# Kernel tuning notes

Hardware: AMD Instinct MI355X
Metric: run time of the kernel (lower is better)

## Reference

```python
import jax, jax.numpy as jnp
import numpy as np

L, B, E, H = 1024, 8, 1024, 16
HD = E // H
SCALE = HD ** -0.5
EPS = 1e-5


def setup_inputs() -> dict:
    key = jax.random.key(0)
    ks = jax.random.split(key, 6)
    s = E ** -0.5
    return {
        "x": jax.random.normal(ks[0], (L, B, E), dtype=jnp.float32),
        "attn_mask": jnp.zeros((L, L), dtype=jnp.float32),
        "Wq": jax.random.normal(ks[1], (E, E), dtype=jnp.float32) * s,
        "bq": jnp.zeros((E,), dtype=jnp.float32),
        "Wk": jax.random.normal(ks[2], (E, E), dtype=jnp.float32) * s,
        "bk": jnp.zeros((E,), dtype=jnp.float32),
        "Wv": jax.random.normal(ks[3], (E, E), dtype=jnp.float32) * s,
        "bv": jnp.zeros((E,), dtype=jnp.float32),
        "Wo": jax.random.normal(ks[4], (E, E), dtype=jnp.float32) * s,
        "bo": jnp.zeros((E,), dtype=jnp.float32),
        "gamma": jnp.ones((E,), dtype=jnp.float32),
        "beta": jnp.zeros((E,), dtype=jnp.float32),
    }


def _layernorm(x, gamma, beta):
    mu = jnp.mean(x, axis=-1, keepdims=True)
    var = jnp.mean(jnp.square(x - mu), axis=-1, keepdims=True)
    return (x - mu) * jax.lax.rsqrt(var + EPS) * gamma + beta


def reference(x, attn_mask, Wq, bq, Wk, bk, Wv, bv, Wo, bo, gamma, beta):
    # x: (L, B, E); pre-LN residual attention block (dropout=0, eval)
    ln_x = _layernorm(x, gamma, beta)
    # torch Linear: y = x @ W.T + b
    q = (ln_x @ Wq.T + bq) * SCALE
    k = ln_x @ Wk.T + bk
    v = ln_x @ Wv.T + bv
    # (L, B, E) -> (B, H, L, hd)
    def split_heads(t):
        return t.reshape(L, B, H, HD).transpose(1, 2, 0, 3)
    q, k, v = split_heads(q), split_heads(k), split_heads(v)
    # full attention matrix, as in the original non-fused bmm path
    attn = jnp.einsum('bhqd,bhkd->bhqk', q, k) + attn_mask[None, None]
    attn = jax.nn.softmax(attn, axis=-1)
    out = jnp.einsum('bhqk,bhkd->bhqd', attn, v)  # (B, H, L, hd)
    out = out.transpose(2, 0, 1, 3).reshape(L, B, E)
    out = out @ Wo.T + bo
    return x + out
```

## Files before the change

### kernel.cpp

```cpp
#include <hip/hip_runtime.h>

#define LL 1024
#define BB 8
#define EE 1024
#define HH 16
#define HD 64
#define MROWS (LL*BB)

typedef __attribute__((ext_vector_type(8))) short short8v;
typedef __attribute__((ext_vector_type(4))) float f32x4;
typedef __attribute__((ext_vector_type(16))) float f32x16;

#define LOG2E 1.44269504088896f

__device__ __forceinline__ unsigned short tobf(float f) {
    union { float f; unsigned u; } un; un.f = f;
    unsigned u = un.u;
    u += 0x7fffu + ((u >> 16) & 1u);
    return (unsigned short)(u >> 16);
}

__device__ __forceinline__ float max3f(float a, float b, float c) {
    return fmaxf(fmaxf(a, b), c);
}

__device__ __forceinline__ void load_lds16(const unsigned short* g, unsigned short* l) {
    __builtin_amdgcn_global_load_lds((const __attribute__((address_space(1))) unsigned int*)g,
                                     (__attribute__((address_space(3))) unsigned int*)l,
                                     16, 0, 0);
}

__global__ __launch_bounds__(256) void convw4_kernel(const float* __restrict__ w0,
                                                     const float* __restrict__ w1,
                                                     const float* __restrict__ w2,
                                                     const float* __restrict__ w3,
                                                     unsigned short* __restrict__ o0,
                                                     unsigned short* __restrict__ o1,
                                                     unsigned short* __restrict__ o2,
                                                     unsigned short* __restrict__ o3) {
    const float* w; unsigned short* o;
    switch (blockIdx.y) {
        case 0:  w = w0; o = o0; break;
        case 1:  w = w1; o = o1; break;
        case 2:  w = w2; o = o2; break;
        default: w = w3; o = o3; break;
    }
    int i = (blockIdx.x * 256 + threadIdx.x) * 4;
    float4 v = *(const float4*)&w[i];
    ushort4 r;
    r.x = tobf(v.x); r.y = tobf(v.y); r.z = tobf(v.z); r.w = tobf(v.w);
    *(ushort4*)&o[i] = r;
}

__global__ __launch_bounds__(256) void maskprep_kernel(const float* __restrict__ m,
                                                       unsigned* __restrict__ o,
                                                       unsigned* __restrict__ flag) {
    __shared__ float t_sh[64][65];
    const int q0 = blockIdx.x * 64, k0 = blockIdx.y * 64;
    const int tid = threadIdx.x;
    unsigned nz = 0;
    {
        const int r = tid >> 2, c0 = (tid & 3) * 16;
        #pragma unroll
        for (int i = 0; i < 4; ++i) {
            float4 v = *(const float4*)&m[(size_t)(q0 + r) * LL + k0 + c0 + i*4];
            nz |= (v.x != 0.0f) | (v.y != 0.0f) | (v.z != 0.0f) | (v.w != 0.0f);
            t_sh[r][c0+i*4+0] = v.x; t_sh[r][c0+i*4+1] = v.y;
            t_sh[r][c0+i*4+2] = v.z; t_sh[r][c0+i*4+3] = v.w;
        }
    }
    if (__any(nz) && (tid & 63) == 0) atomicOr(flag, 1u);
    __syncthreads();
    const int k2l = tid >> 3, qi = (tid & 7) * 8;
    unsigned pk[8];
    #pragma unroll
    for (int j = 0; j < 8; ++j) {
        const unsigned lo = tobf(t_sh[qi+j][2*k2l]   * LOG2E);
        const unsigned hb = tobf(t_sh[qi+j][2*k2l+1] * LOG2E);
        pk[j] = lo | (hb << 16);
    }
    unsigned* orow = &o[(size_t)(k0/2 + k2l) * LL + q0 + qi];
    *(uint4*)&orow[0] = make_uint4(pk[0], pk[1], pk[2], pk[3]);
    *(uint4*)&orow[4] = make_uint4(pk[4], pk[5], pk[6], pk[7]);
}

__global__ __launch_bounds__(256) void ln_kernel(const float* __restrict__ x,
                                                 const float* __restrict__ gamma,
                                                 const float* __restrict__ beta,
                                                 unsigned short* __restrict__ out) {
    const int row = blockIdx.x;
    const int tid = threadIdx.x;
    const float4 v = *(const float4*)&x[(size_t)row * EE + tid * 4];
    float s = v.x + v.y + v.z + v.w;
    float q = v.x*v.x + v.y*v.y + v.z*v.z + v.w*v.w;
    #pragma unroll
    for (int off = 1; off < 64; off <<= 1) {
        s += __shfl_xor(s, off);
        q += __shfl_xor(q, off);
    }
    __shared__ float ss[4], sq[4];
    const int wv = tid >> 6;
    if ((tid & 63) == 0) { ss[wv] = s; sq[wv] = q; }
    __syncthreads();
    s = ss[0] + ss[1] + ss[2] + ss[3];
    q = sq[0] + sq[1] + sq[2] + sq[3];
    const float mu = s * (1.0f / EE);
    const float var = q * (1.0f / EE) - mu * mu;
    const float rs = rsqrtf(var + 1e-5f);
    ushort4 o;
    o.x = tobf((v.x - mu) * rs * gamma[tid*4+0] + beta[tid*4+0]);
    o.y = tobf((v.y - mu) * rs * gamma[tid*4+1] + beta[tid*4+1]);
    o.z = tobf((v.z - mu) * rs * gamma[tid*4+2] + beta[tid*4+2]);
    o.w = tobf((v.w - mu) * rs * gamma[tid*4+3] + beta[tid*4+3]);
    *(ushort4*)&out[(size_t)row * EE + tid * 4] = o;
}

#define GEMM128_BODY(A_, W_)                                                              \
    __shared__ unsigned short a_sh[3][128*32];                                            \
    __shared__ unsigned short b_sh[3][128*32];                                            \
    const int tid = threadIdx.x, lane = tid & 63, wave = tid >> 6;                        \
    const int bm = blockIdx.y * 128, bn = blockIdx.x * 128;                               \
    const int wr = (wave >> 1) * 64, wc = (wave & 1) * 64;                                \
    const int l16 = lane & 15, q4 = lane >> 4;                                            \
    const int grow = lane >> 2;                                                           \
    const int gswz = (((lane & 3) ^ (grow & 3)) * 8);                                     \
    const int rslot = (q4 ^ (l16 & 3)) * 16;                       \
    f32x4 acc[4][4] = {};                                                                 \
    _Pragma("unroll")                                                                     \
    for (int i = 0; i < 2; ++i) {                                                         \
        const int ch = wave * 2 + i;                                                      \
        load_lds16(&A_[(size_t)(bm + ch*16 + grow)*EE + gswz], &a_sh[0][ch*512]);         \
        load_lds16(&W_[(size_t)(bn + ch*16 + grow)*EE + gswz], &b_sh[0][ch*512]);         \
    }                                                                                     \
    _Pragma("unroll")                                                                     \
    for (int i = 0; i < 2; ++i) {                                                         \
        const int ch = wave * 2 + i;                                                      \
        load_lds16(&A_[(size_t)(bm + ch*16 + grow)*EE + 32 + gswz], &a_sh[1][ch*512]);    \
        load_lds16(&W_[(size_t)(bn + ch*16 + grow)*EE + 32 + gswz], &b_sh[1][ch*512]);    \
    }                                                                                     \
    int buf = 0, sb = 2;                                                                  \
    for (int it = 0; it < 32; ++it) {                                                     \
        if (it < 31) asm volatile("s_waitcnt vmcnt(4)" ::: "memory");                     \
        else         asm volatile("s_waitcnt vmcnt(0)" ::: "memory");                     \
        __builtin_amdgcn_s_barrier();                                                     \
        if (it < 30) {                                                                    \
            const int kn = (it + 2) * 32;                                                 \
            _Pragma("unroll")                                                             \
            for (int i = 0; i < 2; ++i) {                                                 \
                const int ch = wave * 2 + i;                                              \
                load_lds16(&A_[(size_t)(bm + ch*16 + grow)*EE + kn + gswz], &a_sh[sb][ch*512]); \
                load_lds16(&W_[(size_t)(bn + ch*16 + grow)*EE + kn + gswz], &b_sh[sb][ch*512]); \
            }                                                                             \
        }                                                                                 \
        short8v af[4], bf[4];                                                             \
        _Pragma("unroll")                                                                 \
        for (int mi = 0; mi < 4; ++mi)                                                    \
            af[mi] = *(const short8v*)((const char*)&a_sh[buf][0] + (size_t)(wr + mi*16 + l16)*64 + rslot); \
        _Pragma("unroll")                                                                 \
        for (int ni = 0; ni < 4; ++ni)                                                    \
            bf[ni] = *(const short8v*)((const char*)&b_sh[buf][0] + (size_t)(wc + ni*16 + l16)*64 + rslot); \
        __builtin_amdgcn_s_setprio(1);                                                    \
        _Pragma("unroll")                                                                 \
        for (int mi = 0; mi < 4; ++mi)                                                    \
            _Pragma("unroll")                                                             \
            for (int ni = 0; ni < 4; ++ni)                                                \
                acc[mi][ni] = __builtin_amdgcn_mfma_f32_16x16x32_bf16(af[mi], bf[ni], acc[mi][ni], 0, 0, 0); \
        __builtin_amdgcn_s_setprio(0);                                                    \
        buf = (buf == 2) ? 0 : buf + 1;                                                   \
        sb  = (sb  == 2) ? 0 : sb  + 1;                                                   \
    }

__global__ __launch_bounds__(256) void gemm_qkv(const unsigned short* __restrict__ A,
                                                const unsigned short* __restrict__ W,
                                                const float* __restrict__ bq,
                                                const float* __restrict__ bk,
                                                const float* __restrict__ bv,
                                                unsigned short* __restrict__ qo,
                                                unsigned short* __restrict__ ko,
                                                unsigned short* __restrict__ vo) {
    GEMM128_BODY(A, W)
    const int seg = blockIdx.x >> 3;
    const float* bias = seg == 0 ? bq : (seg == 1 ? bk : bv);
    #pragma unroll
    for (int mi = 0; mi < 4; ++mi) {
        #pragma unroll
        for (int ni = 0; ni < 4; ++ni) {
            #pragma unroll
            for (int r = 0; r < 4; ++r) {
                const int m  = bm + wr + mi*16 + (lane >> 4)*4 + r;
                const int nn = (bn & 1023) + wc + ni*16 + l16;
                const float v = acc[mi][ni][r] + bias[nn];
                const int l = m >> 3, b = m & 7, h = nn >> 6, d = nn & 63;
                const int bh = b*HH + h;
                if (seg == 2) {
                    const int k16 = l >> 4, khi = (l >> 3) & 1, ke = l & 7;
                    const int dt = d >> 5, dl = d & 31;
                    vo[((((size_t)bh*64 + k16)*2 + dt)*64 + khi*32 + dl)*8 + ke] = tobf(v);
                } else {
                    const int t32 = l >> 5, l32 = l & 31;
                    const int dc = d >> 4, hi2 = (d >> 3) & 1, e = d & 7;
                    const size_t idx = ((((size_t)bh*32 + t32)*4 + dc)*64 + hi2*32 + l32)*8 + e;
                    if (seg == 0) qo[idx] = tobf(v * (0.125f * LOG2E));
                    else          ko[idx] = tobf(v);
                }
            }
        }
    }
}

__global__ __launch_bounds__(256) void gemm_o(const unsigned short* __restrict__ A,
                                              const unsigned short* __restrict__ W,
                                              const float* __restrict__ bias,
                                              const float* __restrict__ xres,
                                              float* __restrict__ outf) {
    GEMM128_BODY(A, W)
    #pragma unroll
    for (int mi = 0; mi < 4; ++mi) {
        #pragma unroll
        for (int ni = 0; ni < 4; ++ni) {
            #pragma unroll
            for (int r = 0; r < 4; ++r) {
                const int m = bm + wr + mi*16 + (lane >> 4)*4 + r;
                const int n = bn + wc + ni*16 + l16;
                outf[(size_t)m * EE + n] = acc[mi][ni][r] + bias[n] + xres[(size_t)m * EE + n];
            }
        }
    }
}

__global__ __launch_bounds__(256, 4) void attn_kernel(const unsigned short* __restrict__ Qf,
                                                      const unsigned short* __restrict__ Kf,
                                                      const unsigned short* __restrict__ Vf,
                                                      const unsigned* __restrict__ maskT2,
                                                      const unsigned* __restrict__ mflagp,
                                                      unsigned short* __restrict__ attn_out) {
    const int tid = threadIdx.x, lane = tid & 63, wave = tid >> 6;
    const int l32 = lane & 31, hi = lane >> 5;
    const int b1 = blockIdx.x;
    const int bh = (b1 & 7) * 16 + ((b1 >> 3) & 15);
    const int qt = ((b1 >> 7) & 7) * 4 + wave;
    const int qtok = qt * 32 + l32;
    const unsigned mf = (unsigned)__builtin_amdgcn_readfirstlane((int)mflagp[0]);
    const unsigned short* qfp = Qf + ((size_t)(bh * 32 + qt) * 4) * 512;
    const unsigned short* kfb = Kf + (size_t)bh * 32 * 4 * 512;
    const unsigned short* vfb = Vf + (size_t)bh * 64 * 2 * 512;

    short8v qf[4];
    #pragma unroll
    for (int dc = 0; dc < 4; ++dc)
        qf[dc] = *(const short8v*)&qfp[dc * 512 + lane * 8];

    union { unsigned u4[4]; short8v s8; } ones;
    #pragma unroll
    for (int i = 0; i < 4; ++i) ones.u4[i] = 0x3F803F80u;

    f32x16 acc[2] = {};
    f32x16 accs = {};
    float mrun = -1e30f;

    const unsigned* mt2base = maskT2 + qtok;
    short8v kf[4];
    #pragma unroll
    for (int dc = 0; dc < 4; ++dc)
        kf[dc] = *(const short8v*)&kfb[dc * 512 + lane * 8];
    unsigned mcur[8], mnxt[8];
    if (mf) {
        #pragma unroll
        for (int j = 0; j < 8; ++j)
            mcur[j] = mt2base[(size_t)((j & 1) + 4*(j >> 1) + 2*hi) * LL];
    }

    for (int t = 0; t < 32; ++t) {
        f32x16 s = {};
        __builtin_amdgcn_s_setprio(1);
        #pragma unroll
        for (int dc = 0; dc < 4; ++dc)
            s = __builtin_amdgcn_mfma_f32_32x32x16_bf16(kf[dc], qf[dc], s, 0, 0, 0);
        __builtin_amdgcn_s_setprio(0);
        short8v vf00, vf01, vf10, vf11;
        vf00 = *(const short8v*)&vfb[((size_t)(t*2 + 0)*2 + 0)*512 + lane*8];
        vf01 = *(const short8v*)&vfb[((size_t)(t*2 + 0)*2 + 1)*512 + lane*8];
        vf10 = *(const short8v*)&vfb[((size_t)(t*2 + 1)*2 + 0)*512 + lane*8];
        vf11 = *(const short8v*)&vfb[((size_t)(t*2 + 1)*2 + 1)*512 + lane*8];
        if (t < 31) {
            #pragma unroll
            for (int dc = 0; dc < 4; ++dc)
                kf[dc] = *(const short8v*)&kfb[((size_t)(t + 1)*4 + dc)*512 + lane*8];
            if (mf) {
                #pragma unroll
                for (int j = 0; j < 8; ++j)
                    mnxt[j] = mt2base[(size_t)((t + 1)*16 + (j & 1) + 4*(j >> 1) + 2*hi) * LL];
            }
        }
        if (mf) {
            #pragma unroll
            for (int j = 0; j < 8; ++j) {
                s[2*j]   += __uint_as_float(mcur[j] << 16);
                s[2*j+1] += __uint_as_float(mcur[j] & 0xffff0000u);
            }
        }
        const float a0 = max3f(s[0],  s[1],  s[2]);
        const float a1 = max3f(s[3],  s[4],  s[5]);
        const float a2 = max3f(s[6],  s[7],  s[8]);
        const float a3 = max3f(s[9],  s[10], s[11]);
        const float a4 = max3f(s[12], s[13], s[14]);
        float pm = fmaxf(max3f(a0, a1, a2), max3f(a3, a4, s[15]));
        {
            float pu = pm, pv = pm;
            asm volatile("v_permlane32_swap_b32 %0, %1" : "+v"(pu), "+v"(pv));
            pm = fmaxf(pu, pv);
        }
        if (__any(pm - mrun > 8.0f)) {
            const float mn = fmaxf(mrun, pm);
            const float al = exp2f(mrun - mn);
            #pragma unroll
            for (int i = 0; i < 16; ++i) { acc[0][i] *= al; acc[1][i] *= al; accs[i] *= al; }
            mrun = mn;
        }
        #pragma unroll
        for (int i = 0; i < 16; ++i) s[i] = exp2f(s[i] - mrun);
        unsigned w[8];
        #pragma unroll
        for (int j = 0; j < 8; ++j)
            asm("v_cvt_pk_bf16_f32 %0, %1, %2" : "=v"(w[j]) : "v"(s[2*j]), "v"(s[2*j+1]));
        asm volatile("v_permlane32_swap_b32 %0, %1" : "+v"(w[0]), "+v"(w[2]));
        asm volatile("v_permlane32_swap_b32 %0, %1" : "+v"(w[1]), "+v"(w[3]));
        asm volatile("v_permlane32_swap_b32 %0, %1" : "+v"(w[4]), "+v"(w[6]));
        asm volatile("v_permlane32_swap_b32 %0, %1" : "+v"(w[5]), "+v"(w[7]));
        union { uint4 u; short8v s8; } pb0, pb1;
        pb0.u = make_uint4(w[0], w[1], w[2], w[3]);
        pb1.u = make_uint4(w[4], w[5], w[6], w[7]);
        __builtin_amdgcn_s_setprio(1);
        accs   = __builtin_amdgcn_mfma_f32_32x32x16_bf16(ones.s8, pb0.s8, accs, 0, 0, 0);
        acc[0] = __builtin_amdgcn_mfma_f32_32x32x16_bf16(vf00, pb0.s8, acc[0], 0, 0, 0);
        acc[1] = __builtin_amdgcn_mfma_f32_32x32x16_bf16(vf01, pb0.s8, acc[1], 0, 0, 0);
        accs   = __builtin_amdgcn_mfma_f32_32x32x16_bf16(ones.s8, pb1.s8, accs, 0, 0, 0);
        acc[0] = __builtin_amdgcn_mfma_f32_32x32x16_bf16(vf10, pb1.s8, acc[0], 0, 0, 0);
        acc[1] = __builtin_amdgcn_mfma_f32_32x32x16_bf16(vf11, pb1.s8, acc[1], 0, 0, 0);
        __builtin_amdgcn_s_setprio(0);
        if (mf) {
            #pragma unroll
            for (int j = 0; j < 8; ++j) mcur[j] = mnxt[j];
        }
    }
    const float inv = 1.0f / accs[0];
    const int b = bh >> 4, h = bh & 15;
    unsigned short* orow = attn_out + ((size_t)qtok * BB + b) * EE + h * HD;
    #pragma unroll
    for (int dt = 0; dt < 2; ++dt) {
        #pragma unroll
        for (int g = 0; g < 4; ++g) {
            const float a0 = acc[dt][4*g+0]*inv, a1 = acc[dt][4*g+1]*inv;
            const float a2 = acc[dt][4*g+2]*inv, a3 = acc[dt][4*g+3]*inv;
            unsigned lo, hw;
            asm("v_cvt_pk_bf16_f32 %0, %1, %2" : "=v"(lo) : "v"(a0), "v"(a1));
            asm("v_cvt_pk_bf16_f32 %0, %1, %2" : "=v"(hw) : "v"(a2), "v"(a3));
            *(uint2*)&orow[dt*32 + g*8 + hi*4] = make_uint2(lo, hw);
        }
    }
}

extern "C" void kernel_launch(void* const* d_in, const int* in_sizes, int n_in,
                              void* d_out, int out_size, void* d_ws, size_t ws_size,
                              hipStream_t stream) {
    (void)in_sizes; (void)n_in; (void)out_size; (void)ws_size;
    const float* x     = (const float*)d_in[0];
    const float* mask  = (const float*)d_in[1];
    const float* Wq    = (const float*)d_in[2];
    const float* bq    = (const float*)d_in[3];
    const float* Wk    = (const float*)d_in[4];
    const float* bk    = (const float*)d_in[5];
    const float* Wv    = (const float*)d_in[6];
    const float* bv    = (const float*)d_in[7];
    const float* Wo    = (const float*)d_in[8];
    const float* bo    = (const float*)d_in[9];
    const float* gamma = (const float*)d_in[10];
    const float* beta  = (const float*)d_in[11];
    float* out = (float*)d_out;

    unsigned short* ws   = (unsigned short*)d_ws;
    unsigned short* ln   = ws;
    unsigned short* wqkv = ln   + (size_t)MROWS * EE;
    unsigned short* wob  = wqkv + (size_t)3 * EE * EE;
    unsigned short* qb   = wob  + (size_t)EE * EE;
    unsigned short* kbp  = qb   + (size_t)BB * HH * LL * HD;
    unsigned short* vtb  = kbp  + (size_t)BB * HH * LL * HD;
    unsigned short* attnb = ln;
    unsigned* maskT2 = (unsigned*)wqkv;
    unsigned* mflag  = (unsigned*)(wqkv + (size_t)2 * EE * EE);

    convw4_kernel<<<dim3(1024, 4), 256, 0, stream>>>(
        Wq, Wk, Wv, Wo,
        wqkv, wqkv + (size_t)EE * EE, wqkv + (size_t)2 * EE * EE, wob);
    ln_kernel<<<MROWS, 256, 0, stream>>>(x, gamma, beta, ln);

    gemm_qkv<<<dim3(24, 64), 256, 0, stream>>>(ln, wqkv, bq, bk, bv, qb, kbp, vtb);

    hipMemsetAsync(mflag, 0, 4, stream);
    maskprep_kernel<<<dim3(16, 16), 256, 0, stream>>>(mask, maskT2, mflag);

    attn_kernel<<<1024, 256, 0, stream>>>(qb, kbp, vtb, maskT2, mflag, attnb);

    gemm_o<<<dim3(8, 64), 256, 0, stream>>>(attnb, wob, bo, x, out);
}
```

Measured before the change: 223.5 us.

## Split attention key range across two waves and merge partial softmax states

The attention kernel now gives each 32-query tile to a 128-thread block of two waves. Each wave processes half of the key tiles and keeps its own running max and sum, and the two partial results are combined through shared memory. The row sum now comes from VALU adds plus a cross-half shuffle instead of extra MFMAs with a ones matrix. This doubles the number of waves in flight and shortens each wave's serial loop, at the cost of a shared-memory merge, a barrier, and one idle wave during the final write.

After: 463.2 us. 2.07x slower.

```diff
diff --git a/kernel.cpp b/kernel.cpp
--- a/kernel.cpp
+++ b/kernel.cpp
@@ -228,17 +228,18 @@
     }
 }
 
-__global__ __launch_bounds__(256, 4) void attn_kernel(const unsigned short* __restrict__ Qf,
+__global__ __launch_bounds__(128, 6) void attn_kernel(const unsigned short* __restrict__ Qf,
                                                       const unsigned short* __restrict__ Kf,
                                                       const unsigned short* __restrict__ Vf,
                                                       const unsigned* __restrict__ maskT2,
                                                       const unsigned* __restrict__ mflagp,
                                                       unsigned short* __restrict__ attn_out) {
-    const int tid = threadIdx.x, lane = tid & 63, wave = tid >> 6;
+    __shared__ float comb[64][34];
+    const int tid = threadIdx.x, lane = tid & 63, kw = tid >> 6;
     const int l32 = lane & 31, hi = lane >> 5;
     const int b1 = blockIdx.x;
     const int bh = (b1 & 7) * 16 + ((b1 >> 3) & 15);
-    const int qt = ((b1 >> 7) & 7) * 4 + wave;
+    const int qt = (b1 >> 7) & 31;
     const int qtok = qt * 32 + l32;
     const unsigned mf = (unsigned)__builtin_amdgcn_readfirstlane((int)mflagp[0]);
     const unsigned short* qfp = Qf + ((size_t)(bh * 32 + qt) * 4) * 512;
@@ -250,27 +251,23 @@
     for (int dc = 0; dc < 4; ++dc)
         qf[dc] = *(const short8v*)&qfp[dc * 512 + lane * 8];
 
-    union { unsigned u4[4]; short8v s8; } ones;
-    #pragma unroll
-    for (int i = 0; i < 4; ++i) ones.u4[i] = 0x3F803F80u;
-
     f32x16 acc[2] = {};
-    f32x16 accs = {};
-    float mrun = -1e30f;
-
+    float mrun = -1e30f, srun = 0.f;
+
+    const int t0 = kw * 16;
     const unsigned* mt2base = maskT2 + qtok;
     short8v kf[4];
     #pragma unroll
     for (int dc = 0; dc < 4; ++dc)
-        kf[dc] = *(const short8v*)&kfb[dc * 512 + lane * 8];
+        kf[dc] = *(const short8v*)&kfb[((size_t)t0 * 4 + dc) * 512 + lane * 8];
     unsigned mcur[8], mnxt[8];
     if (mf) {
         #pragma unroll
         for (int j = 0; j < 8; ++j)
-            mcur[j] = mt2base[(size_t)((j & 1) + 4*(j >> 1) + 2*hi) * LL];
-    }
-
-    for (int t = 0; t < 32; ++t) {
+            mcur[j] = mt2base[(size_t)(t0*16 + (j & 1) + 4*(j >> 1) + 2*hi) * LL];
+    }
+
+    for (int t = t0; t < t0 + 16; ++t) {
         f32x16 s = {};
         __builtin_amdgcn_s_setprio(1);
         #pragma unroll
@@ -282,7 +279,7 @@
         vf01 = *(const short8v*)&vfb[((size_t)(t*2 + 0)*2 + 1)*512 + lane*8];
         vf10 = *(const short8v*)&vfb[((size_t)(t*2 + 1)*2 + 0)*512 + lane*8];
         vf11 = *(const short8v*)&vfb[((size_t)(t*2 + 1)*2 + 1)*512 + lane*8];
-        if (t < 31) {
+        if (t < t0 + 15) {
             #pragma unroll
             for (int dc = 0; dc < 4; ++dc)
                 kf[dc] = *(const short8v*)&kfb[((size_t)(t + 1)*4 + dc)*512 + lane*8];
@@ -305,20 +302,25 @@
         const float a3 = max3f(s[9],  s[10], s[11]);
         const float a4 = max3f(s[12], s[13], s[14]);
         float pm = fmaxf(max3f(a0, a1, a2), max3f(a3, a4, s[15]));
-        {
-            float pu = pm, pv = pm;
-            asm volatile("v_permlane32_swap_b32 %0, %1" : "+v"(pu), "+v"(pv));
-            pm = fmaxf(pu, pv);
-        }
+        pm = fmaxf(pm, __shfl_xor(pm, 32));
         if (__any(pm - mrun > 8.0f)) {
             const float mn = fmaxf(mrun, pm);
             const float al = exp2f(mrun - mn);
             #pragma unroll
-            for (int i = 0; i < 16; ++i) { acc[0][i] *= al; acc[1][i] *= al; accs[i] *= al; }
+            for (int i = 0; i < 16; ++i) { acc[0][i] *= al; acc[1][i] *= al; }
+            srun *= al;
             mrun = mn;
         }
         #pragma unroll
         for (int i = 0; i < 16; ++i) s[i] = exp2f(s[i] - mrun);
+        {
+            const float t0s = s[0]+s[1],  t1s = s[2]+s[3],  t2s = s[4]+s[5],  t3s = s[6]+s[7];
+            const float t4s = s[8]+s[9],  t5s = s[10]+s[11], t6s = s[12]+s[13], t7s = s[14]+s[15];
+            const float u0 = t0s+t1s, u1 = t2s+t3s, u2 = t4s+t5s, u3 = t6s+t7s;
+            float rs = (u0+u1) + (u2+u3);
+            rs += __shfl_xor(rs, 32);
+            srun += rs;
+        }
         unsigned w[8];
         #pragma unroll
         for (int j = 0; j < 8; ++j)
@@ -331,10 +333,8 @@
         pb0.u = make_uint4(w[0], w[1], w[2], w[3]);
         pb1.u = make_uint4(w[4], w[5], w[6], w[7]);
         __builtin_amdgcn_s_setprio(1);
-        accs   = __builtin_amdgcn_mfma_f32_32x32x16_bf16(ones.s8, pb0.s8, accs, 0, 0, 0);
         acc[0] = __builtin_amdgcn_mfma_f32_32x32x16_bf16(vf00, pb0.s8, acc[0], 0, 0, 0);
         acc[1] = __builtin_amdgcn_mfma_f32_32x32x16_bf16(vf01, pb0.s8, acc[1], 0, 0, 0);
-        accs   = __builtin_amdgcn_mfma_f32_32x32x16_bf16(ones.s8, pb1.s8, accs, 0, 0, 0);
         acc[0] = __builtin_amdgcn_mfma_f32_32x32x16_bf16(vf10, pb1.s8, acc[0], 0, 0, 0);
         acc[1] = __builtin_amdgcn_mfma_f32_32x32x16_bf16(vf11, pb1.s8, acc[1], 0, 0, 0);
         __builtin_amdgcn_s_setprio(0);
@@ -343,19 +343,36 @@
             for (int j = 0; j < 8; ++j) mcur[j] = mnxt[j];
         }
     }
-    const float inv = 1.0f / accs[0];
-    const int b = bh >> 4, h = bh & 15;
-    unsigned short* orow = attn_out + ((size_t)qtok * BB + b) * EE + h * HD;
-    #pragma unroll
-    for (int dt = 0; dt < 2; ++dt) {
-        #pragma unroll
-        for (int g = 0; g < 4; ++g) {
-            const float a0 = acc[dt][4*g+0]*inv, a1 = acc[dt][4*g+1]*inv;
-            const float a2 = acc[dt][4*g+2]*inv, a3 = acc[dt][4*g+3]*inv;
-            unsigned lo, hw;
-            asm("v_cvt_pk_bf16_f32 %0, %1, %2" : "=v"(lo) : "v"(a0), "v"(a1));
-            asm("v_cvt_pk_bf16_f32 %0, %1, %2" : "=v"(hw) : "v"(a2), "v"(a3));
-            *(uint2*)&orow[dt*32 + g*8 + hi*4] = make_uint2(lo, hw);
+    if (kw == 1) {
+        #pragma unroll
+        for (int i = 0; i < 16; ++i) {
+            comb[lane][i]      = acc[0][i];
+            comb[lane][16 + i] = acc[1][i];
+        }
+        comb[lane][32] = mrun;
+        comb[lane][33] = srun;
+    }
+    __syncthreads();
+    if (kw == 0) {
+        const float m1 = comb[lane][32], s1 = comb[lane][33];
+        const float M  = fmaxf(mrun, m1);
+        const float c0 = exp2f(mrun - M), c1 = exp2f(m1 - M);
+        const float inv = 1.0f / (srun * c0 + s1 * c1);
+        const int b = bh >> 4, h = bh & 15;
+        unsigned short* orow = attn_out + ((size_t)qtok * BB + b) * EE + h * HD;
+        #pragma unroll
+        for (int dt = 0; dt < 2; ++dt) {
+            #pragma unroll
+            for (int g = 0; g < 4; ++g) {
+                const float o0 = (acc[dt][4*g+0]*c0 + comb[lane][dt*16 + 4*g+0]*c1) * inv;
+                const float o1 = (acc[dt][4*g+1]*c0 + comb[lane][dt*16 + 4*g+1]*c1) * inv;
+                const float o2 = (acc[dt][4*g+2]*c0 + comb[lane][dt*16 + 4*g+2]*c1) * inv;
+                const float o3 = (acc[dt][4*g+3]*c0 + comb[lane][dt*16 + 4*g+3]*c1) * inv;
+                unsigned lo, hw;
+                asm("v_cvt_pk_bf16_f32 %0, %1, %2" : "=v"(lo) : "v"(o0), "v"(o1));
+                asm("v_cvt_pk_bf16_f32 %0, %1, %2" : "=v"(hw) : "v"(o2), "v"(o3));
+                *(uint2*)&orow[dt*32 + g*8 + hi*4] = make_uint2(lo, hw);
+            }
         }
     }
 }
@@ -399,7 +416,7 @@
     hipMemsetAsync(mflag, 0, 4, stream);
     maskprep_kernel<<<dim3(16, 16), 256, 0, stream>>>(mask, maskT2, mflag);
 
-    attn_kernel<<<1024, 256, 0, stream>>>(qb, kbp, vtb, maskT2, mflag, attnb);
+    attn_kernel<<<4096, 128, 0, stream>>>(qb, kbp, vtb, maskT2, mflag, attnb);
 
     gemm_o<<<dim3(8, 64), 256, 0, stream>>>(attnb, wob, bo, x, out);
 }
```

## Software-pipeline QK^T one tile ahead and compute row sums with VALU

Applied to the files above, without the earlier changes.

The attention loop now issues the QK^T MFMAs for tile t while running the softmax and PV MFMAs for tile t-1, so matrix work overlaps the exp and max work. The row sum is no longer built by extra MFMAs against a ones vector. It is summed in f32 on the VALU with a cross-half shuffle and rescaled alongside the accumulators. This adds a second score register set and more mask registers, which raises register pressure and may lower occupancy.

Measured after the change: 245.3 us. +9.8%, slower.

```diff
diff --git a/kernel.cpp b/kernel.cpp
--- a/kernel.cpp
+++ b/kernel.cpp
@@ -250,53 +250,31 @@
     for (int dc = 0; dc < 4; ++dc)
         qf[dc] = *(const short8v*)&qfp[dc * 512 + lane * 8];
 
-    union { unsigned u4[4]; short8v s8; } ones;
-    #pragma unroll
-    for (int i = 0; i < 4; ++i) ones.u4[i] = 0x3F803F80u;
-
     f32x16 acc[2] = {};
-    f32x16 accs = {};
-    float mrun = -1e30f;
+    float mrun = -1e30f, srun = 0.f;
 
     const unsigned* mt2base = maskT2 + qtok;
     short8v kf[4];
     #pragma unroll
     for (int dc = 0; dc < 4; ++dc)
         kf[dc] = *(const short8v*)&kfb[dc * 512 + lane * 8];
-    unsigned mcur[8], mnxt[8];
+    unsigned mprev[8], mcur[8];
     if (mf) {
         #pragma unroll
         for (int j = 0; j < 8; ++j)
-            mcur[j] = mt2base[(size_t)((j & 1) + 4*(j >> 1) + 2*hi) * LL];
-    }
-
-    for (int t = 0; t < 32; ++t) {
-        f32x16 s = {};
-        __builtin_amdgcn_s_setprio(1);
-        #pragma unroll
-        for (int dc = 0; dc < 4; ++dc)
-            s = __builtin_amdgcn_mfma_f32_32x32x16_bf16(kf[dc], qf[dc], s, 0, 0, 0);
-        __builtin_amdgcn_s_setprio(0);
-        short8v vf00, vf01, vf10, vf11;
-        vf00 = *(const short8v*)&vfb[((size_t)(t*2 + 0)*2 + 0)*512 + lane*8];
-        vf01 = *(const short8v*)&vfb[((size_t)(t*2 + 0)*2 + 1)*512 + lane*8];
-        vf10 = *(const short8v*)&vfb[((size_t)(t*2 + 1)*2 + 0)*512 + lane*8];
-        vf11 = *(const short8v*)&vfb[((size_t)(t*2 + 1)*2 + 1)*512 + lane*8];
-        if (t < 31) {
-            #pragma unroll
-            for (int dc = 0; dc < 4; ++dc)
-                kf[dc] = *(const short8v*)&kfb[((size_t)(t + 1)*4 + dc)*512 + lane*8];
-            if (mf) {
-                #pragma unroll
-                for (int j = 0; j < 8; ++j)
-                    mnxt[j] = mt2base[(size_t)((t + 1)*16 + (j & 1) + 4*(j >> 1) + 2*hi) * LL];
-            }
-        }
+            mprev[j] = mt2base[(size_t)((j & 1) + 4*(j >> 1) + 2*hi) * LL];
+    }
+
+    auto finish = [&](f32x16& s, const unsigned* mu, int tf) {
+        const short8v vf00 = *(const short8v*)&vfb[((size_t)(tf*2 + 0)*2 + 0)*512 + lane*8];
+        const short8v vf01 = *(const short8v*)&vfb[((size_t)(tf*2 + 0)*2 + 1)*512 + lane*8];
+        const short8v vf10 = *(const short8v*)&vfb[((size_t)(tf*2 + 1)*2 + 0)*512 + lane*8];
+        const short8v vf11 = *(const short8v*)&vfb[((size_t)(tf*2 + 1)*2 + 1)*512 + lane*8];
         if (mf) {
             #pragma unroll
             for (int j = 0; j < 8; ++j) {
-                s[2*j]   += __uint_as_float(mcur[j] << 16);
-                s[2*j+1] += __uint_as_float(mcur[j] & 0xffff0000u);
+                s[2*j]   += __uint_as_float(mu[j] << 16);
+                s[2*j+1] += __uint_as_float(mu[j] & 0xffff0000u);
             }
         }
         const float a0 = max3f(s[0],  s[1],  s[2]);
@@ -305,20 +283,25 @@
         const float a3 = max3f(s[9],  s[10], s[11]);
         const float a4 = max3f(s[12], s[13], s[14]);
         float pm = fmaxf(max3f(a0, a1, a2), max3f(a3, a4, s[15]));
-        {
-            float pu = pm, pv = pm;
-            asm volatile("v_permlane32_swap_b32 %0, %1" : "+v"(pu), "+v"(pv));
-            pm = fmaxf(pu, pv);
-        }
+        pm = fmaxf(pm, __shfl_xor(pm, 32));
         if (__any(pm - mrun > 8.0f)) {
             const float mn = fmaxf(mrun, pm);
             const float al = exp2f(mrun - mn);
             #pragma unroll
-            for (int i = 0; i < 16; ++i) { acc[0][i] *= al; acc[1][i] *= al; accs[i] *= al; }
+            for (int i = 0; i < 16; ++i) { acc[0][i] *= al; acc[1][i] *= al; }
+            srun *= al;
             mrun = mn;
         }
         #pragma unroll
         for (int i = 0; i < 16; ++i) s[i] = exp2f(s[i] - mrun);
+        {
+            const float t0s = s[0]+s[1],  t1s = s[2]+s[3],  t2s = s[4]+s[5],  t3s = s[6]+s[7];
+            const float t4s = s[8]+s[9],  t5s = s[10]+s[11], t6s = s[12]+s[13], t7s = s[14]+s[15];
+            const float u0 = t0s+t1s, u1 = t2s+t3s, u2 = t4s+t5s, u3 = t6s+t7s;
+            float rs = (u0+u1) + (u2+u3);
+            rs += __shfl_xor(rs, 32);
+            srun += rs;
+        }
         unsigned w[8];
         #pragma unroll
         for (int j = 0; j < 8; ++j)
@@ -331,19 +314,56 @@
         pb0.u = make_uint4(w[0], w[1], w[2], w[3]);
         pb1.u = make_uint4(w[4], w[5], w[6], w[7]);
         __builtin_amdgcn_s_setprio(1);
-        accs   = __builtin_amdgcn_mfma_f32_32x32x16_bf16(ones.s8, pb0.s8, accs, 0, 0, 0);
         acc[0] = __builtin_amdgcn_mfma_f32_32x32x16_bf16(vf00, pb0.s8, acc[0], 0, 0, 0);
         acc[1] = __builtin_amdgcn_mfma_f32_32x32x16_bf16(vf01, pb0.s8, acc[1], 0, 0, 0);
-        accs   = __builtin_amdgcn_mfma_f32_32x32x16_bf16(ones.s8, pb1.s8, accs, 0, 0, 0);
         acc[0] = __builtin_amdgcn_mfma_f32_32x32x16_bf16(vf10, pb1.s8, acc[0], 0, 0, 0);
         acc[1] = __builtin_amdgcn_mfma_f32_32x32x16_bf16(vf11, pb1.s8, acc[1], 0, 0, 0);
         __builtin_amdgcn_s_setprio(0);
+    };
+
+    f32x16 s_prev = {};
+    __builtin_amdgcn_s_setprio(1);
+    #pragma unroll
+    for (int dc = 0; dc < 4; ++dc)
+        s_prev = __builtin_amdgcn_mfma_f32_32x32x16_bf16(kf[dc], qf[dc], s_prev, 0, 0, 0);
+    __builtin_amdgcn_s_setprio(0);
+    #pragma unroll
+    for (int dc = 0; dc < 4; ++dc)
+        kf[dc] = *(const short8v*)&kfb[((size_t)4 + dc)*512 + lane*8];
+    if (mf) {
+        #pragma unroll
+        for (int j = 0; j < 8; ++j)
+            mcur[j] = mt2base[(size_t)(16 + (j & 1) + 4*(j >> 1) + 2*hi) * LL];
+    }
+
+    for (int t = 1; t < 32; ++t) {
+        f32x16 s_cur = {};
+        __builtin_amdgcn_s_setprio(1);
+        #pragma unroll
+        for (int dc = 0; dc < 4; ++dc)
+            s_cur = __builtin_amdgcn_mfma_f32_32x32x16_bf16(kf[dc], qf[dc], s_cur, 0, 0, 0);
+        __builtin_amdgcn_s_setprio(0);
+        unsigned mnxt[8];
+        if (t < 31) {
+            #pragma unroll
+            for (int dc = 0; dc < 4; ++dc)
+                kf[dc] = *(const short8v*)&kfb[((size_t)(t + 1)*4 + dc)*512 + lane*8];
+            if (mf) {
+                #pragma unroll
+                for (int j = 0; j < 8; ++j)
+                    mnxt[j] = mt2base[(size_t)((t + 1)*16 + (j & 1) + 4*(j >> 1) + 2*hi) * LL];
+            }
+        }
+        finish(s_prev, mprev, t - 1);
+        s_prev = s_cur;
         if (mf) {
             #pragma unroll
-            for (int j = 0; j < 8; ++j) mcur[j] = mnxt[j];
-        }
-    }
-    const float inv = 1.0f / accs[0];
+            for (int j = 0; j < 8; ++j) { mprev[j] = mcur[j]; mcur[j] = mnxt[j]; }
+        }
+    }
+    finish(s_prev, mprev, 31);
+
+    const float inv = 1.0f / srun;
     const int b = bh >> 4, h = bh & 15;
     unsigned short* orow = attn_out + ((size_t)qtok * BB + b) * EE + h * HD;
     #pragma unroll
```
